# Kernel tuning notes

Measured on AMD Instinct MI355X. Metric: run time of the kernel, lower is better.

The kernel has to match this reference:

```python
import jax, jax.numpy as jnp
import numpy as np

B, T, C = 4, 1024, 1024
HS = 64                 # head_size_a
H = C // HS             # 16 heads
H_KV = 4                # num_key_value_heads
N_REP = H // H_KV       # GQA repeat factor
D_DECAY = 64            # max(32, round(1.8*sqrt(1024)/32)*32)
D_MV = 32               # max(32, round(1.3*sqrt(1024)/32)*32)
LAYER_ID = 1
N_LAYER = 24
EPS = 0.00064


def setup_inputs() -> dict:
    key = jax.random.key(0)
    ks = jax.random.split(key, 16)
    def nrm(k, shape, s):
        return jax.random.normal(k, shape, jnp.float32) * s
    ratio_0_to_1 = LAYER_ID / (N_LAYER - 1)
    n = np.arange(C, dtype=np.float64)
    decay_speed = -7.0 + 5.0 * (n / (C - 1)) ** (0.85 + 1.0 * ratio_0_to_1 ** 0.5)
    return dict(
        x=nrm(ks[0], (B, T, C), 1.0),
        v_first=nrm(ks[1], (B, T, C), 1.0),
        attention_mask=jnp.ones((B, T), jnp.float32),
        Wr=nrm(ks[2], (H * HS, C), C ** -0.5),
        Wk=nrm(ks[3], (H_KV * HS, C), C ** -0.5),
        Wv=nrm(ks[4], (H_KV * HS, C), C ** -0.5),
        Wo=nrm(ks[5], (C, H * HS), C ** -0.5),
        w0=jnp.asarray(decay_speed + 0.5, jnp.float32),
        w1=nrm(ks[6], (C, D_DECAY), 0.02),
        w2=nrm(ks[7], (D_DECAY, C), 0.02),
        a0=jnp.zeros((C,), jnp.float32),
        a1=nrm(ks[8], (C, D_DECAY), 0.02),
        a2=nrm(ks[9], (D_DECAY, C), 0.02),
        v0=jnp.ones((C,), jnp.float32),
        v1=nrm(ks[10], (C, D_MV), 0.02),
        v2=nrm(ks[11], (D_MV, C), 0.02),
        k_k=jnp.full((C,), 0.85, jnp.float32),
        k_a=jnp.ones((C,), jnp.float32),
        r_k=nrm(ks[12], (H, HS), 0.02),
        ln_g=jnp.ones((C,), jnp.float32),
        ln_b=jnp.zeros((C,), jnp.float32),
    )


def _wkv7(r, w, k, v, a, b, mask):
    """RWKV-7 delta-rule recurrence. r,w,k,v,a,b: (B,T,C); mask: (B,T).
    State S: (B,H,N_value,N_key). Per step:
      S = S * exp(-exp(w)) + (S @ a) b^T + v k^T ;  y = S @ r
    """
    Bx, Tx, Cx = r.shape
    def rs(t):  # (B,T,C) -> (T,B,H,N)
        return t.reshape(Bx, Tx, H, HS).transpose(1, 0, 2, 3)
    decay = jnp.exp(-jnp.exp(w))
    m = mask.T[:, :, None, None]  # (T,B,1,1)
    rT, dT, kT, vT, aT, bT = map(rs, (r, decay, k, v, a, b))
    kT = kT * m; vT = vT * m; aT = aT * m; bT = bT * m
    dT = jnp.where(m > 0, dT, 1.0)  # masked steps leave state untouched

    def step(S, inp):
        r_t, d_t, k_t, v_t, a_t, b_t = inp  # each (B,H,N)
        sa = jnp.einsum('bhij,bhj->bhi', S, a_t)
        S = S * d_t[:, :, None, :] + sa[..., None] * b_t[:, :, None, :] \
            + v_t[..., None] * k_t[:, :, None, :]
        y = jnp.einsum('bhij,bhj->bhi', S, r_t)
        return S, y

    S0 = jnp.zeros((Bx, H, HS, HS), r.dtype)
    _, yT = jax.lax.scan(step, S0, (rT, dT, kT, vT, aT, bT))
    return yT.transpose(1, 0, 2, 3).reshape(Bx, Tx, Cx)


def reference(x, v_first, attention_mask, Wr, Wk, Wv, Wo, w0, w1, w2,
              a0, a1, a2, v0, v1, v2, k_k, k_a, r_k, ln_g, ln_b):
    B_, T_, C_ = x.shape
    r = x @ Wr.T
    w = -jax.nn.softplus(-(w0 + jnp.tanh(x @ w1) @ w2)) - 0.6
    k = x @ Wk.T  # (B,T,H_KV*HS)
    v = x @ Wv.T

    def rep(t):  # GQA repeat_kv: (B,T,H_kv*N) -> (B,T,H*N)
        t = t.reshape(B_, T_, H_KV, 1, HS)
        return jnp.broadcast_to(t, (B_, T_, H_KV, N_REP, HS)).reshape(B_, T_, C_)
    k = rep(k); v = rep(v)

    # layer_id != 0: residual mix with first layer's v
    v = v + (v_first - v) * jax.nn.sigmoid(v0 + x @ v1 @ v2)
    a = jax.nn.sigmoid(a0 + x @ a1 @ a2)

    kk = (k * k_k).reshape(B_, T_, H, HS)
    kk = kk / jnp.maximum(jnp.linalg.norm(kk, axis=-1, keepdims=True), 1e-12)
    kk = kk.reshape(B_, T_, C_)
    k = k * (1.0 + (a - 1.0) * k_a)

    y = _wkv7(r, w, k, v, -kk, kk * a, attention_mask)

    # GroupNorm(H, C): per-head normalization over HS channels
    yh = y.reshape(B_, T_, H, HS)
    mu = yh.mean(-1, keepdims=True)
    var = yh.var(-1, keepdims=True)
    y = ((yh - mu) / jnp.sqrt(var + EPS)).reshape(B_, T_, C_) * ln_g + ln_b

    rk = (r.reshape(B_, T_, H, HS) * k.reshape(B_, T_, H, HS) * r_k).sum(-1, keepdims=True)
    y = y + (rk * v.reshape(B_, T_, H, HS)).reshape(B_, T_, C_)
    out = y @ Wo.T
    return (out, v_first)
```

## Files before the change

### kernel.cpp

```cpp
#include <hip/hip_runtime.h>


#define NROWS 4096
#define CCH   1024
#define EPSV  0.00064f

typedef __attribute__((ext_vector_type(4))) float f32x4;
typedef __attribute__((ext_vector_type(8))) short bf16x8;

__device__ __forceinline__ unsigned short f2b(float f) {
    unsigned x = __float_as_uint(f);
    return (unsigned short)((x + 0x7fffu + ((x >> 16) & 1u)) >> 16);
}
__device__ __forceinline__ float b2f(unsigned short u) {
    return __uint_as_float(((unsigned)u) << 16);
}

#define LDSTR 40

template<bool TANH>
__global__ __launch_bounds__(256) void gemm_split(
    const float* __restrict__ A, int lda, const float* __restrict__ B, int ldb,
    float* __restrict__ C, int ldc, int M, int N, int K, int tl, int th)
{
    __shared__ __align__(16) unsigned short Ah[128 * LDSTR];
    __shared__ __align__(16) unsigned short Al[128 * LDSTR];
    __shared__ __align__(16) unsigned short Bh[128 * LDSTR];
    __shared__ __align__(16) unsigned short Bl[128 * LDSTR];
    const int t = threadIdx.x;
    const int wave = t >> 6, lane = t & 63;
    const int m0 = blockIdx.y * 128, n0 = blockIdx.x * 128;
    const int wm = (wave >> 1) * 64, wn = (wave & 1) * 64;
    const int fr = lane & 15, kq = lane >> 4;

    f32x4 acc[4][4];
    #pragma unroll
    for (int i = 0; i < 4; ++i)
        #pragma unroll
        for (int j = 0; j < 4; ++j)
            acc[i][j] = (f32x4){0.f, 0.f, 0.f, 0.f};

    const int srow = t >> 3;
    const int scol = (t & 7) * 4;

    for (int k0 = 0; k0 < K; k0 += 32) {
        #pragma unroll
        for (int p = 0; p < 4; ++p) {
            const int row = p * 32 + srow;
            {
                const float4 v = *reinterpret_cast<const float4*>(
                    A + (size_t)(m0 + row) * lda + k0 + scol);
                ushort4 h, l;
                h.x = f2b(v.x); l.x = f2b(v.x - b2f(h.x));
                h.y = f2b(v.y); l.y = f2b(v.y - b2f(h.y));
                h.z = f2b(v.z); l.z = f2b(v.z - b2f(h.z));
                h.w = f2b(v.w); l.w = f2b(v.w - b2f(h.w));
                *reinterpret_cast<ushort4*>(&Ah[row * LDSTR + scol]) = h;
                *reinterpret_cast<ushort4*>(&Al[row * LDSTR + scol]) = l;
            }
            {
                float4 v = make_float4(0.f, 0.f, 0.f, 0.f);
                if (n0 + row < N)
                    v = *reinterpret_cast<const float4*>(
                        B + (size_t)(n0 + row) * ldb + k0 + scol);
                ushort4 h, l;
                h.x = f2b(v.x); l.x = f2b(v.x - b2f(h.x));
                h.y = f2b(v.y); l.y = f2b(v.y - b2f(h.y));
                h.z = f2b(v.z); l.z = f2b(v.z - b2f(h.z));
                h.w = f2b(v.w); l.w = f2b(v.w - b2f(h.w));
                *reinterpret_cast<ushort4*>(&Bh[row * LDSTR + scol]) = h;
                *reinterpret_cast<ushort4*>(&Bl[row * LDSTR + scol]) = l;
            }
        }
        __syncthreads();

        bf16x8 ah[4], al[4], bh[4], bl[4];
        #pragma unroll
        for (int mi = 0; mi < 4; ++mi) {
            ah[mi] = *reinterpret_cast<const bf16x8*>(&Ah[(wm + mi * 16 + fr) * LDSTR + kq * 8]);
            al[mi] = *reinterpret_cast<const bf16x8*>(&Al[(wm + mi * 16 + fr) * LDSTR + kq * 8]);
        }
        #pragma unroll
        for (int ni = 0; ni < 4; ++ni) {
            bh[ni] = *reinterpret_cast<const bf16x8*>(&Bh[(wn + ni * 16 + fr) * LDSTR + kq * 8]);
            bl[ni] = *reinterpret_cast<const bf16x8*>(&Bl[(wn + ni * 16 + fr) * LDSTR + kq * 8]);
        }
        #pragma unroll
        for (int mi = 0; mi < 4; ++mi)
            #pragma unroll
            for (int ni = 0; ni < 4; ++ni) {
                acc[mi][ni] = __builtin_amdgcn_mfma_f32_16x16x32_bf16(
                    al[mi], bh[ni], acc[mi][ni], 0, 0, 0);
                acc[mi][ni] = __builtin_amdgcn_mfma_f32_16x16x32_bf16(
                    ah[mi], bl[ni], acc[mi][ni], 0, 0, 0);
                acc[mi][ni] = __builtin_amdgcn_mfma_f32_16x16x32_bf16(
                    ah[mi], bh[ni], acc[mi][ni], 0, 0, 0);
            }
        __syncthreads();
    }

    const int crow0 = m0 + wm + kq * 4;
    const int ccol0 = n0 + wn + fr;
    #pragma unroll
    for (int mi = 0; mi < 4; ++mi)
        #pragma unroll
        for (int ni = 0; ni < 4; ++ni) {
            const int col = ccol0 + ni * 16;
            if (col < N) {
                #pragma unroll
                for (int i = 0; i < 4; ++i) {
                    float v = acc[mi][ni][i];
                    if (TANH && col >= tl && col < th) v = tanhf(v);
                    C[(size_t)(crow0 + mi * 16 + i) * ldc + col] = v;
                }
            }
        }
}

__global__ __launch_bounds__(256) void gemm_mfma(
    const float* __restrict__ A, int lda, const float* __restrict__ B, int ldb,
    float* __restrict__ C, int ldc, int M, int N, int K)
{
    __shared__ __align__(16) unsigned short Ah[128 * LDSTR];
    __shared__ __align__(16) unsigned short Bh[128 * LDSTR];
    const int t = threadIdx.x;
    const int wave = t >> 6, lane = t & 63;
    const int m0 = blockIdx.y * 128, n0 = blockIdx.x * 128;
    const int wm = (wave >> 1) * 64, wn = (wave & 1) * 64;
    const int fr = lane & 15, kq = lane >> 4;

    f32x4 acc[4][4];
    #pragma unroll
    for (int i = 0; i < 4; ++i)
        #pragma unroll
        for (int j = 0; j < 4; ++j)
            acc[i][j] = (f32x4){0.f, 0.f, 0.f, 0.f};

    const int srow = t >> 3;
    const int scol = (t & 7) * 4;

    for (int k0 = 0; k0 < K; k0 += 32) {
        #pragma unroll
        for (int p = 0; p < 4; ++p) {
            const int row = p * 32 + srow;
            const float4 av = *reinterpret_cast<const float4*>(
                A + (size_t)(m0 + row) * lda + k0 + scol);
            ushort4 a4;
            a4.x = f2b(av.x); a4.y = f2b(av.y); a4.z = f2b(av.z); a4.w = f2b(av.w);
            *reinterpret_cast<ushort4*>(&Ah[row * LDSTR + scol]) = a4;
            const float4 bv = *reinterpret_cast<const float4*>(
                B + (size_t)(n0 + row) * ldb + k0 + scol);
            ushort4 b4;
            b4.x = f2b(bv.x); b4.y = f2b(bv.y); b4.z = f2b(bv.z); b4.w = f2b(bv.w);
            *reinterpret_cast<ushort4*>(&Bh[row * LDSTR + scol]) = b4;
        }
        __syncthreads();

        bf16x8 af[4], bfr[4];
        #pragma unroll
        for (int mi = 0; mi < 4; ++mi)
            af[mi] = *reinterpret_cast<const bf16x8*>(&Ah[(wm + mi * 16 + fr) * LDSTR + kq * 8]);
        #pragma unroll
        for (int ni = 0; ni < 4; ++ni)
            bfr[ni] = *reinterpret_cast<const bf16x8*>(&Bh[(wn + ni * 16 + fr) * LDSTR + kq * 8]);
        #pragma unroll
        for (int mi = 0; mi < 4; ++mi)
            #pragma unroll
            for (int ni = 0; ni < 4; ++ni)
                acc[mi][ni] = __builtin_amdgcn_mfma_f32_16x16x32_bf16(
                    af[mi], bfr[ni], acc[mi][ni], 0, 0, 0);
        __syncthreads();
    }

    const int crow0 = m0 + wm + kq * 4;
    const int ccol0 = n0 + wn + fr;
    #pragma unroll
    for (int mi = 0; mi < 4; ++mi)
        #pragma unroll
        for (int ni = 0; ni < 4; ++ni) {
            const int col = ccol0 + ni * 16;
            #pragma unroll
            for (int i = 0; i < 4; ++i)
                C[(size_t)(crow0 + mi * 16 + i) * ldc + col] = acc[mi][ni][i];
        }
}

__global__ __launch_bounds__(256) void gemm_stage2(
    const float* __restrict__ kvh,
    const float* __restrict__ w2T, const float* __restrict__ a2T,
    const float* __restrict__ v2T,
    float* __restrict__ wdec, float* __restrict__ kf, float* __restrict__ vf)
{
    const int z = blockIdx.z;
    const float* A = kvh + (z == 0 ? 512 : z == 1 ? 576 : 640);
    const float* B = z == 0 ? w2T : z == 1 ? a2T : v2T;
    float* C       = z == 0 ? wdec : z == 1 ? kf : vf;
    const int K    = z == 2 ? 32 : 64;
    const int ldb  = K;

    __shared__ __align__(16) unsigned short Ah[128 * LDSTR];
    __shared__ __align__(16) unsigned short Bh[128 * LDSTR];
    const int t = threadIdx.x;
    const int wave = t >> 6, lane = t & 63;
    const int m0 = blockIdx.y * 128, n0 = blockIdx.x * 128;
    const int wm = (wave >> 1) * 64, wn = (wave & 1) * 64;
    const int fr = lane & 15, kq = lane >> 4;

    f32x4 acc[4][4];
    #pragma unroll
    for (int i = 0; i < 4; ++i)
        #pragma unroll
        for (int j = 0; j < 4; ++j)
            acc[i][j] = (f32x4){0.f, 0.f, 0.f, 0.f};

    const int srow = t >> 3;
    const int scol = (t & 7) * 4;

    for (int k0 = 0; k0 < K; k0 += 32) {
        #pragma unroll
        for (int p = 0; p < 4; ++p) {
            const int row = p * 32 + srow;
            const float4 av = *reinterpret_cast<const float4*>(
                A + (size_t)(m0 + row) * 672 + k0 + scol);
            ushort4 a4;
            a4.x = f2b(av.x); a4.y = f2b(av.y); a4.z = f2b(av.z); a4.w = f2b(av.w);
            *reinterpret_cast<ushort4*>(&Ah[row * LDSTR + scol]) = a4;
            const float4 bv = *reinterpret_cast<const float4*>(
                B + (size_t)(n0 + row) * ldb + k0 + scol);
            ushort4 b4;
            b4.x = f2b(bv.x); b4.y = f2b(bv.y); b4.z = f2b(bv.z); b4.w = f2b(bv.w);
            *reinterpret_cast<ushort4*>(&Bh[row * LDSTR + scol]) = b4;
        }
        __syncthreads();

        bf16x8 af[4], bfr[4];
        #pragma unroll
        for (int mi = 0; mi < 4; ++mi)
            af[mi] = *reinterpret_cast<const bf16x8*>(&Ah[(wm + mi * 16 + fr) * LDSTR + kq * 8]);
        #pragma unroll
        for (int ni = 0; ni < 4; ++ni)
            bfr[ni] = *reinterpret_cast<const bf16x8*>(&Bh[(wn + ni * 16 + fr) * LDSTR + kq * 8]);
        #pragma unroll
        for (int mi = 0; mi < 4; ++mi)
            #pragma unroll
            for (int ni = 0; ni < 4; ++ni)
                acc[mi][ni] = __builtin_amdgcn_mfma_f32_16x16x32_bf16(
                    af[mi], bfr[ni], acc[mi][ni], 0, 0, 0);
        __syncthreads();
    }

    const int crow0 = m0 + wm + kq * 4;
    const int ccol0 = n0 + wn + fr;
    #pragma unroll
    for (int mi = 0; mi < 4; ++mi)
        #pragma unroll
        for (int ni = 0; ni < 4; ++ni) {
            const int col = ccol0 + ni * 16;
            #pragma unroll
            for (int i = 0; i < 4; ++i)
                C[(size_t)(crow0 + mi * 16 + i) * 1024 + col] = acc[mi][ni][i];
        }
}

__global__ __launch_bounds__(256) void pack_all(
    const float* __restrict__ Wk, const float* __restrict__ Wv,
    const float* __restrict__ w1, const float* __restrict__ a1,
    const float* __restrict__ v1, const float* __restrict__ w2,
    const float* __restrict__ a2, const float* __restrict__ v2,
    float* __restrict__ Wkvh,
    float* __restrict__ w2T, float* __restrict__ a2T, float* __restrict__ v2T)
{
    const int blk = blockIdx.x, t = threadIdx.x;
    if (blk < 512) {
        const float* s = blk < 256 ? Wk + (size_t)blk * 1024
                                   : Wv + (size_t)(blk - 256) * 1024;
        const float4 v = *reinterpret_cast<const float4*>(s + t * 4);
        *reinterpret_cast<float4*>(Wkvh + (size_t)blk * 1024 + t * 4) = v;
    } else if (blk < 672) {
        const int f = blk - 512;
        for (int c = t; c < 1024; c += 256) {
            float val;
            if (f < 64)       val = w1[c * 64 + f];
            else if (f < 128) val = a1[c * 64 + (f - 64)];
            else              val = v1[c * 32 + (f - 128)];
            Wkvh[(size_t)(512 + f) * 1024 + c] = val;
        }
    } else {
        const int c = blk - 672;
        if (t < 64)       w2T[c * 64 + t]         = w2[t * 1024 + c];
        else if (t < 128) a2T[c * 64 + (t - 64)]  = a2[(t - 64) * 1024 + c];
        else if (t < 160) v2T[c * 32 + (t - 128)] = v2[(t - 128) * 1024 + c];
    }
}

__global__ __launch_bounds__(256) void fuse_pre(
    const float* __restrict__ kvh,
    const float* __restrict__ v_first, const float* __restrict__ mask,
    const float* __restrict__ w0, const float* __restrict__ a0,
    const float* __restrict__ v0,
    const float* __restrict__ k_k, const float* __restrict__ k_a,
    float* __restrict__ wdec, float* __restrict__ kf, float* __restrict__ vf,
    float* __restrict__ aab, float* __restrict__ bbb)
{
    const int n = blockIdx.x, t = threadIdx.x;
    const float m = mask[n];
    const bool live = m > 0.f;

    #pragma unroll
    for (int q = 0; q < 4; ++q) {
        const int c = q * 256 + t;
        const size_t idx = (size_t)n * 1024 + c;
        const float dd   = w0[c] + wdec[idx];
        const float aacc = a0[c] + kf[idx];
        const float vacc = v0[c] + vf[idx];

        const float u  = -dd;
        const float sp = fmaxf(u, 0.f) + log1pf(expf(-fabsf(u)));
        const float dec = expf(-expf(-sp - 0.6f));
        const float av = 1.f / (1.f + expf(-aacc));
        const float sv = 1.f / (1.f + expf(-vacc));

        const int  ck  = q * 64 + (c & 63);
        const float kr = kvh[(size_t)n * 672 + ck];
        const float vr = kvh[(size_t)n * 672 + 256 + ck];
        const float vfi = v_first[idx];
        const float vv  = vr + (vfi - vr) * sv;

        const float tkk = kr * k_k[c];
        float ss = tkk * tkk;
        #pragma unroll
        for (int off = 32; off > 0; off >>= 1) ss += __shfl_xor(ss, off, 64);
        const float kkv = tkk / fmaxf(sqrtf(ss), 1e-12f);

        wdec[idx] = live ? dec : 1.f;
        kf[idx]   = kr * (1.f + (av - 1.f) * k_a[c]) * m;
        vf[idx]   = vv * m;
        aab[idx]  = -kkv * m;
        bbb[idx]  = kkv * av * m;
    }
}

__device__ __forceinline__ float qred16(float x) {
    x += __int_as_float(__builtin_amdgcn_update_dpp(
        0, __float_as_int(x), 0xB1, 0xF, 0xF, true));
    x += __int_as_float(__builtin_amdgcn_update_dpp(
        0, __float_as_int(x), 0x4E, 0xF, 0xF, true));
    x += __int_as_float(__builtin_amdgcn_update_dpp(
        0, __float_as_int(x), 0x141, 0xF, 0xF, true));
    x += __int_as_float(__builtin_amdgcn_update_dpp(
        0, __float_as_int(x), 0x140, 0xF, 0xF, true));
    return x;
}

__global__ __launch_bounds__(256, 1) void wkv7(
    const float* __restrict__ r, const float* __restrict__ wdec,
    const float* __restrict__ kf, const float* __restrict__ vf,
    const float* __restrict__ aab, const float* __restrict__ bbb,
    float* __restrict__ y)
{
    const int blk = blockIdx.x;
    const int m  = blk & 7;
    const int s  = blk >> 3;
    const int bh = (s >> 2) * 8 + m;
    const int j  = s & 3;
    const int b = bh >> 4, h = bh & 15;
    const int wave = threadIdx.x >> 6;
    const int lane = threadIdx.x & 63;
    const int li   = lane & 15;
    const int i    = j * 16 + wave * 4 + (lane >> 4);
    const int c0   = li * 4;
    const size_t cb = (size_t)b * (1024 * 1024) + (size_t)h * 64;

    float4 S = make_float4(0.f, 0.f, 0.f, 0.f);

    float4 dA, kA, aA, bA, rA; float vA;
    float4 dB, kB, aB, bB, rB; float vB;

#define LD(T, d_, k_, a_, b_, r_, v_)                                   \
    {   const size_t p_ = cb + (size_t)(T) * 1024;                      \
        d_ = *reinterpret_cast<const float4*>(wdec + p_ + c0);          \
        k_ = *reinterpret_cast<const float4*>(kf   + p_ + c0);          \
        a_ = *reinterpret_cast<const float4*>(aab  + p_ + c0);          \
        b_ = *reinterpret_cast<const float4*>(bbb  + p_ + c0);          \
        r_ = *reinterpret_cast<const float4*>(r    + p_ + c0);          \
        v_ = vf[p_ + i]; }

#define STEP(d_, k_, a_, b_, r_, v_, YOUT)                              \
    {   float sa_ = S.x * a_.x + S.y * a_.y + S.z * a_.z + S.w * a_.w;  \
        sa_ = qred16(sa_);                                              \
        S.x = S.x * d_.x + sa_ * b_.x + v_ * k_.x;                     \
        S.y = S.y * d_.y + sa_ * b_.y + v_ * k_.y;                     \
        S.z = S.z * d_.z + sa_ * b_.z + v_ * k_.z;                     \
        S.w = S.w * d_.w + sa_ * b_.w + v_ * k_.w;                     \
        float yv_ = S.x * r_.x + S.y * r_.y + S.z * r_.z + S.w * r_.w; \
        YOUT = qred16(yv_); }

    LD(0, dA, kA, aA, bA, rA, vA);
    LD(1, dB, kB, aB, bB, rB, vB);

    for (int t = 0; t < 1024; t += 2) {
        float y0, y1;
        const int t2 = t + 2 < 1024 ? t + 2 : 1023;
        const int t3 = t + 3 < 1024 ? t + 3 : 1023;
        STEP(dA, kA, aA, bA, rA, vA, y0);
        LD(t2, dA, kA, aA, bA, rA, vA);
        STEP(dB, kB, aB, bB, rB, vB, y1);
        LD(t3, dB, kB, aB, bB, rB, vB);
        if (li == 0) {
            const size_t yb = cb + (size_t)t * 1024 + i;
            y[yb]        = y0;
            y[yb + 1024] = y1;
        }
    }
#undef LD
#undef STEP
}

__global__ __launch_bounds__(256) void fuse_post(
    const float* __restrict__ y, const float* __restrict__ r,
    const float* __restrict__ kf, const float* __restrict__ vf,
    const float* __restrict__ r_k, const float* __restrict__ ln_g, const float* __restrict__ ln_b,
    float* __restrict__ yn)
{
    const int n = blockIdx.x, t = threadIdx.x;
    #pragma unroll
    for (int q = 0; q < 4; ++q) {
        const int c = q * 256 + t;
        const size_t idx = (size_t)n * 1024 + c;
        const float yv = y[idx];
        float s1 = yv, s2 = yv * yv;
        float rk = r[idx] * kf[idx] * r_k[c];
        #pragma unroll
        for (int off = 32; off > 0; off >>= 1) {
            s1 += __shfl_xor(s1, off, 64);
            s2 += __shfl_xor(s2, off, 64);
            rk += __shfl_xor(rk, off, 64);
        }
        const float mu  = s1 * (1.f / 64.f);
        const float var = s2 * (1.f / 64.f) - mu * mu;
        yn[idx] = (yv - mu) * rsqrtf(var + EPSV) * ln_g[c] + ln_b[c]
                  + rk * vf[idx];
    }
}

extern "C" void kernel_launch(void* const* d_in, const int* in_sizes, int n_in,
                              void* d_out, int out_size, void* d_ws, size_t ws_size,
                              hipStream_t stream)
{
    const float* x       = (const float*)d_in[0];
    const float* v_first = (const float*)d_in[1];
    const float* mask    = (const float*)d_in[2];
    const float* Wr      = (const float*)d_in[3];
    const float* Wk      = (const float*)d_in[4];
    const float* Wv      = (const float*)d_in[5];
    const float* Wo      = (const float*)d_in[6];
    const float* w0      = (const float*)d_in[7];
    const float* w1      = (const float*)d_in[8];
    const float* w2      = (const float*)d_in[9];
    const float* a0      = (const float*)d_in[10];
    const float* a1      = (const float*)d_in[11];
    const float* a2      = (const float*)d_in[12];
    const float* v0      = (const float*)d_in[13];
    const float* v1      = (const float*)d_in[14];
    const float* v2      = (const float*)d_in[15];
    const float* k_k     = (const float*)d_in[16];
    const float* k_a     = (const float*)d_in[17];
    const float* r_k     = (const float*)d_in[18];
    const float* ln_g    = (const float*)d_in[19];
    const float* ln_b    = (const float*)d_in[20];
    float* out = (float*)d_out;

    float* ws = (float*)d_ws;
    const size_t M4 = (size_t)NROWS * CCH;
    float* rbuf = ws;
    float* wdec = ws + 1 * M4;
    float* kf   = ws + 2 * M4;
    float* vf   = ws + 3 * M4;
    float* aab  = ws + 4 * M4;
    float* bbb  = ws + 5 * M4;
    float* ybuf = ws + 6 * M4;
    float* kvh  = ybuf;
    float* w2T  = kvh  + (size_t)NROWS * 672;
    float* a2T  = w2T  + (size_t)1024 * 64;
    float* v2T  = a2T  + (size_t)1024 * 64;
    float* Wkvh = v2T  + (size_t)1024 * 32;
    float* yn = aab;

    dim3 blk(256);
    pack_all<<<1696, blk, 0, stream>>>(Wk, Wv, w1, a1, v1, w2, a2, v2,
                                       Wkvh, w2T, a2T, v2T);
    gemm_mfma<<<dim3(8, 32), blk, 0, stream>>>(
        x, 1024, Wr, 1024, rbuf, 1024, NROWS, 1024, 1024);
    gemm_split<true><<<dim3(6, 32), blk, 0, stream>>>(
        x, 1024, Wkvh, 1024, kvh, 672, NROWS, 672, 1024, 512, 576);
    gemm_stage2<<<dim3(8, 32, 3), blk, 0, stream>>>(
        kvh, w2T, a2T, v2T, wdec, kf, vf);
    fuse_pre<<<NROWS, blk, 0, stream>>>(kvh, v_first, mask, w0, a0, v0,
                                        k_k, k_a, wdec, kf, vf, aab, bbb);
    wkv7<<<256, blk, 0, stream>>>(rbuf, wdec, kf, vf, aab, bbb, ybuf);
    fuse_post<<<NROWS, blk, 0, stream>>>(ybuf, rbuf, kf, vf, r_k, ln_g, ln_b, yn);
    gemm_mfma<<<dim3(8, 32), blk, 0, stream>>>(
        yn, 1024, Wo, 1024, out, 1024, NROWS, 1024, 1024);
    hipMemcpyAsync(out + M4, v_first, M4 * sizeof(float),
                   hipMemcpyDeviceToDevice, stream);
}
```

Before: 542.0 us.

## Stage WKV7 step inputs through double-buffered LDS with async global-to-LDS loads

The recurrence kernel now copies 8 timesteps of decay, k, a, b, r and v into shared memory with global_load_lds, double-buffered, instead of each thread issuing per-step float4 register loads two steps ahead. The aim is to remove redundant per-wave global loads, since all four waves of a block read the same key-dimension data, and to hide memory latency behind 8 steps of compute. The cost is a block barrier and a manual vmcnt wait every 8 steps. The vmcnt(8) count has to match the number of outstanding stores and loads exactly, which is fragile.

Measured after the change: 492.5 us (median of 2 runs). 1.1x faster.

```diff
diff --git a/kernel.cpp b/kernel.cpp
--- a/kernel.cpp
+++ b/kernel.cpp
@@ -358,62 +358,87 @@
     const float* __restrict__ aab, const float* __restrict__ bbb,
     float* __restrict__ y)
 {
+    __shared__ __align__(16) float4 sl[2][672];
     const int blk = blockIdx.x;
     const int m  = blk & 7;
-    const int s  = blk >> 3;
-    const int bh = (s >> 2) * 8 + m;
-    const int j  = s & 3;
+    const int s_ = blk >> 3;
+    const int bh = (s_ >> 2) * 8 + m;
+    const int j  = s_ & 3;
     const int b = bh >> 4, h = bh & 15;
-    const int wave = threadIdx.x >> 6;
-    const int lane = threadIdx.x & 63;
+    const int tid  = threadIdx.x;
+    const int wave = tid >> 6;
+    const int lane = tid & 63;
     const int li   = lane & 15;
-    const int i    = j * 16 + wave * 4 + (lane >> 4);
-    const int c0   = li * 4;
+    const int il   = wave * 4 + (lane >> 4);
+    const int i    = j * 16 + il;
     const size_t cb = (size_t)b * (1024 * 1024) + (size_t)h * 64;
 
-    float4 S = make_float4(0.f, 0.f, 0.f, 0.f);
-
-    float4 dA, kA, aA, bA, rA; float vA;
-    float4 dB, kB, aB, bB, rB; float vB;
-
-#define LD(T, d_, k_, a_, b_, r_, v_)                                   \
-    {   const size_t p_ = cb + (size_t)(T) * 1024;                      \
-        d_ = *reinterpret_cast<const float4*>(wdec + p_ + c0);          \
-        k_ = *reinterpret_cast<const float4*>(kf   + p_ + c0);          \
-        a_ = *reinterpret_cast<const float4*>(aab  + p_ + c0);          \
-        b_ = *reinterpret_cast<const float4*>(bbb  + p_ + c0);          \
-        r_ = *reinterpret_cast<const float4*>(r    + p_ + c0);          \
-        v_ = vf[p_ + i]; }
-
-#define STEP(d_, k_, a_, b_, r_, v_, YOUT)                              \
-    {   float sa_ = S.x * a_.x + S.y * a_.y + S.z * a_.z + S.w * a_.w;  \
-        sa_ = qred16(sa_);                                              \
-        S.x = S.x * d_.x + sa_ * b_.x + v_ * k_.x;                     \
-        S.y = S.y * d_.y + sa_ * b_.y + v_ * k_.y;                     \
-        S.z = S.z * d_.z + sa_ * b_.z + v_ * k_.z;                     \
-        S.w = S.w * d_.w + sa_ * b_.w + v_ * k_.w;                     \
-        float yv_ = S.x * r_.x + S.y * r_.y + S.z * r_.z + S.w * r_.w; \
-        YOUT = qred16(yv_); }
-
-    LD(0, dA, kA, aA, bA, rA, vA);
-    LD(1, dB, kB, aB, bB, rB, vB);
-
-    for (int t = 0; t < 1024; t += 2) {
-        float y0, y1;
-        const int t2 = t + 2 < 1024 ? t + 2 : 1023;
-        const int t3 = t + 3 < 1024 ? t + 3 : 1023;
-        STEP(dA, kA, aA, bA, rA, vA, y0);
-        LD(t2, dA, kA, aA, bA, rA, vA);
-        STEP(dB, kB, aB, bB, rB, vB, y1);
-        LD(t3, dB, kB, aB, bB, rB, vB);
-        if (li == 0) {
-            const size_t yb = cb + (size_t)t * 1024 + i;
-            y[yb]        = y0;
-            y[yb + 1024] = y1;
-        }
-    }
-#undef LD
-#undef STEP
+#define GLL16(g, l) __builtin_amdgcn_global_load_lds( \
+        (const __attribute__((address_space(1))) unsigned int*)(g), \
+        (__attribute__((address_space(3))) unsigned int*)(l), 16, 0, 0)
+
+    auto stage = [&](int t0, int bf) {
+        #pragma unroll
+        for (int k = 0; k < 3; ++k) {
+            const int q = tid + k * 256;
+            if (q < 672) {
+                const float* gp;
+                if (q < 640) {
+                    const int s  = q / 80;
+                    const int rm = q - s * 80;
+                    const int arr = rm >> 4, c16 = rm & 15;
+                    const float* base = arr == 0 ? wdec : arr == 1 ? kf
+                                      : arr == 2 ? aab : arr == 3 ? bbb : r;
+                    gp = base + cb + (size_t)(t0 + s) * 1024 + c16 * 4;
+                } else {
+                    const int qq = q - 640;
+                    const int s = qq >> 2, c4 = qq & 3;
+                    gp = vf + cb + (size_t)(t0 + s) * 1024 + j * 16 + c4 * 4;
+                }
+                GLL16(gp, &sl[bf][wave * 64 + k * 256]);
+            }
+        }
+    };
+
+    float4 S = (float4){0.f, 0.f, 0.f, 0.f};
+
+    stage(0, 0);
+    asm volatile("s_waitcnt vmcnt(0)" ::: "memory");
+    __builtin_amdgcn_sched_barrier(0);
+    __builtin_amdgcn_s_barrier();
+
+    for (int g = 0; g < 128; ++g) {
+        const int bf = g & 1;
+        const int t0 = g * 8;
+        if (g + 1 < 128) stage(t0 + 8, bf ^ 1);
+        __builtin_amdgcn_sched_barrier(0);
+
+        #pragma unroll
+        for (int s = 0; s < 8; ++s) {
+            const float4 d4 = sl[bf][s * 80 + 0  + li];
+            const float4 k4 = sl[bf][s * 80 + 16 + li];
+            const float4 a4 = sl[bf][s * 80 + 32 + li];
+            const float4 b4 = sl[bf][s * 80 + 48 + li];
+            const float4 r4 = sl[bf][s * 80 + 64 + li];
+            const float  vv = reinterpret_cast<const float*>(
+                                  &sl[bf][640 + s * 4])[il];
+
+            float sa = S.x * a4.x + S.y * a4.y + S.z * a4.z + S.w * a4.w;
+            sa = qred16(sa);
+            S.x = S.x * d4.x + sa * b4.x + vv * k4.x;
+            S.y = S.y * d4.y + sa * b4.y + vv * k4.y;
+            S.z = S.z * d4.z + sa * b4.z + vv * k4.z;
+            S.w = S.w * d4.w + sa * b4.w + vv * k4.w;
+            float yv = S.x * r4.x + S.y * r4.y + S.z * r4.z + S.w * r4.w;
+            yv = qred16(yv);
+            if (li == 0) y[cb + (size_t)(t0 + s) * 1024 + i] = yv;
+        }
+
+        asm volatile("s_waitcnt vmcnt(8)" ::: "memory");
+        __builtin_amdgcn_sched_barrier(0);
+        __builtin_amdgcn_s_barrier();
+    }
+#undef GLL16
 }
 
 __global__ __launch_bounds__(256) void fuse_post(
```
